# Optimization experiments

Hardware: AMD Instinct MI355X
Metric: run time of the kernel (lower is better)

Reference implementation:

```python
import jax, jax.numpy as jnp
import numpy as np
import math

B, L, D = 4, 4096, 64

def setup_inputs() -> dict:
    key = jax.random.key(0)
    kq, kk, kv = jax.random.split(key, 3)
    q = jax.random.normal(kq, (B, L, D), dtype=jnp.float32)
    k = jax.random.normal(kk, (B, L, D), dtype=jnp.float32)
    v = jax.random.normal(kv, (B, L, D), dtype=jnp.float32)
    return {"q": q, "k": k, "v": v}

def reference(q, k, v):
    d_model = k.shape[-1]
    # score[b,i,j] = <q_i, k_j> / sqrt(d)   -> [B, L, L]
    score = jnp.einsum('bid,bjd->bij', q, k) / math.sqrt(d_model)
    attn = jax.nn.softmax(score.astype(jnp.float32), axis=-1)
    # Faithful to source: output = (v^T @ attn)^T = attn^T @ v
    # output[b,j,d] = sum_i attn[b,i,j] * v[b,i,d]
    out = jnp.einsum('bij,bid->bjd', attn, v)
    return out
```

## Files before the change

kernel.cpp:

```cpp
#include <hip/hip_runtime.h>
#include <hip/hip_bf16.h>

#define LQ 4096
#define DD 64
#define NB 4
#define NTOT ((size_t)NB * LQ * DD)
#define NROW ((size_t)NB * LQ)

typedef __attribute__((ext_vector_type(4))) float f32x4;
typedef __attribute__((ext_vector_type(8))) short short8;
typedef __attribute__((ext_vector_type(2))) unsigned int uint2v;
typedef __attribute__((ext_vector_type(4))) unsigned short ushort4v;

static __device__ __forceinline__ unsigned short f2bf(float x) {
  __hip_bfloat16 h = __float2bfloat16(x);
  return __builtin_bit_cast(unsigned short, h);
}
static __device__ __forceinline__ float bf2f(unsigned short u) {
  unsigned int v = ((unsigned int)u) << 16;
  return __builtin_bit_cast(float, v);
}
static __device__ __forceinline__ float ex2(float x) { return __builtin_amdgcn_exp2f(x); }

static __device__ __forceinline__ void gl_lds16(const unsigned short* g, unsigned short* l) {
  __builtin_amdgcn_global_load_lds(
      (const __attribute__((address_space(1))) unsigned int*)g,
      (__attribute__((address_space(3))) unsigned int*)l, 16, 0, 0);
}

#define C1 0.18033688011112042f

__global__ __launch_bounds__(256) void prep_kernel(
    const float* __restrict__ q, const float* __restrict__ k,
    const float* __restrict__ v,
    unsigned short* __restrict__ Qb, unsigned short* __restrict__ Kb,
    unsigned short* __restrict__ Vb)
{
  const int arr = blockIdx.x >> 9;
  const size_t off = (((size_t)(blockIdx.x & 511)) * 256 + threadIdx.x) * 8;
  const float* s = arr == 0 ? q : arr == 1 ? k : v;
  unsigned short* d = arr == 0 ? Qb : arr == 1 ? Kb : Vb;
  const f32x4 x0 = *(const f32x4*)(s + off);
  const f32x4 x1 = *(const f32x4*)(s + off + 4);
  ushort4v o0 = { f2bf(x0[0]), f2bf(x0[1]), f2bf(x0[2]), f2bf(x0[3]) };
  ushort4v o1 = { f2bf(x1[0]), f2bf(x1[1]), f2bf(x1[2]), f2bf(x1[3]) };
  *(ushort4v*)(d + off) = o0;
  *(ushort4v*)(d + off + 4) = o1;
}

__global__ __launch_bounds__(256, 2) void stats_kernel(
    const unsigned short* __restrict__ Qb, const unsigned short* __restrict__ Kb,
    float* __restrict__ part_ls)
{
  __shared__ __align__(16) unsigned short stK[3][2048];
  const int bx = blockIdx.x;
  const int jc = bx & 7, it = (bx >> 3) & 15, b = bx >> 7;
  const int tid = threadIdx.x, w = tid >> 6, lane = tid & 63;
  const int l15 = lane & 15, g = lane >> 4;
  const int i0 = it * 256 + w * 64;
  const int jbase = jc * 512;
  const unsigned short* Kbase = Kb + (size_t)b * LQ * DD;

  short8 aq[4][2];
#pragma unroll
  for (int is = 0; is < 4; ++is)
#pragma unroll
    for (int kh = 0; kh < 2; ++kh)
      aq[is][kh] = *(const short8*)(Qb + ((size_t)b * LQ + i0 + is * 16 + l15) * DD + kh * 32 + g * 8);

  float ls[4][4];
#pragma unroll
  for (int is = 0; is < 4; ++is)
#pragma unroll
    for (int qq = 0; qq < 4; ++qq) ls[is][qq] = 0.f;

  const int srow = w * 8 + (lane >> 3);
  const int scol = ((lane & 7) ^ (lane >> 3)) << 3;

  gl_lds16(Kbase + (size_t)(jbase + srow) * DD + scol, &stK[0][w * 512]);
  gl_lds16(Kbase + (size_t)(jbase + 32 + srow) * DD + scol, &stK[1][w * 512]);
  asm volatile("s_waitcnt vmcnt(1)" ::: "memory");
  __builtin_amdgcn_s_barrier();

  for (int itr = 0; itr < 16; ++itr) {
    const int cur = itr % 3;
    const int tn = (itr + 2 < 16) ? itr + 2 : 15;
    gl_lds16(Kbase + (size_t)(jbase + tn * 32 + srow) * DD + scol, &stK[(itr + 2) % 3][w * 512]);

    short8 kf[2][2];
#pragma unroll
    for (int jsub = 0; jsub < 2; ++jsub)
#pragma unroll
      for (int kh = 0; kh < 2; ++kh) {
        const int row = jsub * 16 + l15;
        kf[jsub][kh] = *(const short8*)(&stK[cur][row * 64 + (((kh * 4 + g) ^ (l15 & 7)) << 3)]);
      }
#pragma unroll
    for (int is = 0; is < 4; ++is)
#pragma unroll
      for (int jsub = 0; jsub < 2; ++jsub) {
        f32x4 tt = __builtin_amdgcn_mfma_f32_16x16x32_bf16(
            aq[is][0], kf[jsub][0], (f32x4){0.f, 0.f, 0.f, 0.f}, 0, 0, 0);
        tt = __builtin_amdgcn_mfma_f32_16x16x32_bf16(aq[is][1], kf[jsub][1], tt, 0, 0, 0);
#pragma unroll
        for (int qq = 0; qq < 4; ++qq) ls[is][qq] += ex2(tt[qq] * C1);
      }
    asm volatile("s_waitcnt vmcnt(1)" ::: "memory");
    __builtin_amdgcn_s_barrier();
  }
#pragma unroll
  for (int mask = 1; mask <= 8; mask <<= 1)
#pragma unroll
    for (int is = 0; is < 4; ++is)
#pragma unroll
      for (int qq = 0; qq < 4; ++qq) ls[is][qq] += __shfl_xor(ls[is][qq], mask, 64);
  if (l15 == 0) {
#pragma unroll
    for (int is = 0; is < 4; ++is)
#pragma unroll
      for (int qq = 0; qq < 4; ++qq)
        part_ls[(size_t)jc * NROW + b * LQ + i0 + is * 16 + g * 4 + qq] = ls[is][qq];
  }
}

__global__ __launch_bounds__(256) void combine_kernel(
    const float* __restrict__ part_ls, const unsigned short* __restrict__ Vb,
    unsigned short* __restrict__ Vs)
{
  const size_t base = ((size_t)blockIdx.x * 256 + threadIdx.x) * 8;
  const int r = (int)(base >> 6);
  float l = 0.f;
#pragma unroll
  for (int jc = 0; jc < 8; ++jc) l += part_ls[(size_t)jc * NROW + r];
  const float s = 1.0f / l;
  const ushort4v a = *(const ushort4v*)(Vb + base);
  const ushort4v c = *(const ushort4v*)(Vb + base + 4);
  ushort4v oa = { f2bf(bf2f(a[0]) * s), f2bf(bf2f(a[1]) * s),
                  f2bf(bf2f(a[2]) * s), f2bf(bf2f(a[3]) * s) };
  ushort4v oc = { f2bf(bf2f(c[0]) * s), f2bf(bf2f(c[1]) * s),
                  f2bf(bf2f(c[2]) * s), f2bf(bf2f(c[3]) * s) };
  *(ushort4v*)(Vs + base) = oa;
  *(ushort4v*)(Vs + base + 4) = oc;
}

__global__ __launch_bounds__(1024, 4) void attn_out_kernel(
    const unsigned short* __restrict__ Qb, const unsigned short* __restrict__ Kb,
    const unsigned short* __restrict__ Vs, float* __restrict__ out)
{
  __shared__ __align__(16) unsigned short stage[16][4096];
  __shared__ __align__(16) unsigned short Pall[16 * 544];

  const int bx = blockIdx.x;
  const int jt = bx & 63;
  const int b  = bx >> 6;
  const int tid = threadIdx.x, w = tid >> 6, lane = tid & 63;
  const int p = w >> 1, sub = w & 1;
  const int l15 = lane & 15, g = lane >> 4;
  const int j0 = jt * 64 + sub * 32;

  const unsigned short* Qbase = Qb + (size_t)b * LQ * DD;
  const unsigned short* Vbase = Vs + (size_t)b * LQ * DD;

  short8 ka[2][2];
#pragma unroll
  for (int jsl = 0; jsl < 2; ++jsl)
#pragma unroll
    for (int kh = 0; kh < 2; ++kh)
      ka[jsl][kh] = *(const short8*)(Kb + ((size_t)b * LQ + j0 + jsl * 16 + l15) * DD + kh * 32 + g * 8);

  f32x4 acc[2][4];
#pragma unroll
  for (int jsl = 0; jsl < 2; ++jsl)
#pragma unroll
    for (int ds = 0; ds < 4; ++ds) acc[jsl][ds] = (f32x4){0.f, 0.f, 0.f, 0.f};

  const int ibase = p * 512;
  const int qrow = lane >> 3;
  const int qcol = ((lane & 7) ^ (lane >> 3)) << 3;
  const int vrow = (lane >> 5) * 4 + ((lane >> 1) & 3);
  const int vcol = (((lane >> 3) & 3) << 4) + ((lane & 1) << 3);

  unsigned short* Pw = &Pall[w * 544];
  const unsigned pbyte = (unsigned)(size_t)Pw;
  const unsigned sbyte = (unsigned)(size_t)&stage[w][0];

#define STAGE(I0) do { \
    _Pragma("unroll") \
    for (int kk = 0; kk < 4; ++kk) { \
      gl_lds16(Qbase + (size_t)((I0) + kk * 8 + qrow) * DD + qcol, &stage[w][kk * 512]); \
      gl_lds16(Vbase + (size_t)((I0) + kk * 8 + vrow) * DD + vcol, &stage[w][2048 + kk * 512]); \
    } \
  } while (0)

  STAGE(ibase);
  asm volatile("s_waitcnt vmcnt(0)" ::: "memory");

  for (int itr = 0; itr < 16; ++itr) {
    short8 qf[2][2];
#pragma unroll
    for (int is = 0; is < 2; ++is)
#pragma unroll
      for (int kh = 0; kh < 2; ++kh) {
        const int row = is * 16 + l15;
        qf[is][kh] = *(const short8*)(&stage[w][row * 64 + (((kh * 4 + g) ^ (l15 & 7)) << 3)]);
      }

    unsigned long long v0, v1, v2, v3, v4, v5, v6, v7;
    const unsigned av = sbyte + 4096 + g * 1024 + l15 * 8;
    asm volatile(
        "ds_read_b64_tr_b16 %0, %8\n\t"
        "ds_read_b64_tr_b16 %1, %8 offset:512\n\t"
        "ds_read_b64_tr_b16 %2, %8 offset:128\n\t"
        "ds_read_b64_tr_b16 %3, %8 offset:640\n\t"
        "ds_read_b64_tr_b16 %4, %8 offset:256\n\t"
        "ds_read_b64_tr_b16 %5, %8 offset:768\n\t"
        "ds_read_b64_tr_b16 %6, %8 offset:384\n\t"
        "ds_read_b64_tr_b16 %7, %8 offset:896\n\t"
        "s_waitcnt lgkmcnt(0)"
        : "=&v"(v0), "=&v"(v1), "=&v"(v2), "=&v"(v3),
          "=&v"(v4), "=&v"(v5), "=&v"(v6), "=&v"(v7)
        : "v"(av) : "memory");
    union U { unsigned long long u[2]; short8 s; };
    U vf0, vf1, vf2, vf3;
    vf0.u[0] = v0; vf0.u[1] = v1;
    vf1.u[0] = v2; vf1.u[1] = v3;
    vf2.u[0] = v4; vf2.u[1] = v5;
    vf3.u[0] = v6; vf3.u[1] = v7;

    if (itr + 1 < 16) STAGE(ibase + (itr + 1) * 32);

#pragma unroll
    for (int jsl = 0; jsl < 2; ++jsl) {
      __builtin_amdgcn_s_setprio(1);
#pragma unroll
      for (int is = 0; is < 2; ++is) {
        f32x4 tt = __builtin_amdgcn_mfma_f32_16x16x32_bf16(
            ka[jsl][0], qf[is][0], (f32x4){0.f, 0.f, 0.f, 0.f}, 0, 0, 0);
        tt = __builtin_amdgcn_mfma_f32_16x16x32_bf16(ka[jsl][1], qf[is][1], tt, 0, 0, 0);
        const unsigned a0 = __builtin_bit_cast(unsigned, ex2(tt[0] * C1)) + 0x8000u;
        const unsigned a1 = __builtin_bit_cast(unsigned, ex2(tt[1] * C1)) + 0x8000u;
        const unsigned a2 = __builtin_bit_cast(unsigned, ex2(tt[2] * C1)) + 0x8000u;
        const unsigned a3 = __builtin_bit_cast(unsigned, ex2(tt[3] * C1)) + 0x8000u;
        uint2v uu;
        uu[0] = __builtin_amdgcn_perm(a1, a0, 0x07060302u);
        uu[1] = __builtin_amdgcn_perm(a3, a2, 0x07060302u);
        const int il = is * 16 + l15;
        *(uint2v*)(&Pw[(il >> 2) * 68 + (il & 3) * 16 + g * 4]) = uu;
      }
      __builtin_amdgcn_s_setprio(0);

      unsigned long long p0, p1;
      const unsigned ap = pbyte + g * 272 + l15 * 8;
      asm volatile(
          "s_waitcnt lgkmcnt(0)\n\t"
          "ds_read_b64_tr_b16 %0, %2\n\t"
          "ds_read_b64_tr_b16 %1, %2 offset:136\n\t"
          "s_waitcnt lgkmcnt(0)"
          : "=&v"(p0), "=&v"(p1)
          : "v"(ap) : "memory");
      U pa;
      pa.u[0] = p0; pa.u[1] = p1;
      __builtin_amdgcn_s_setprio(1);
      acc[jsl][0] = __builtin_amdgcn_mfma_f32_16x16x32_bf16(pa.s, vf0.s, acc[jsl][0], 0, 0, 0);
      acc[jsl][1] = __builtin_amdgcn_mfma_f32_16x16x32_bf16(pa.s, vf1.s, acc[jsl][1], 0, 0, 0);
      acc[jsl][2] = __builtin_amdgcn_mfma_f32_16x16x32_bf16(pa.s, vf2.s, acc[jsl][2], 0, 0, 0);
      acc[jsl][3] = __builtin_amdgcn_mfma_f32_16x16x32_bf16(pa.s, vf3.s, acc[jsl][3], 0, 0, 0);
      __builtin_amdgcn_s_setprio(0);
    }

    asm volatile("s_waitcnt vmcnt(0)" ::: "memory");
  }
#undef STAGE

  __syncthreads();
  float* red = (float*)&stage[0][0];
#pragma unroll
  for (int jsl = 0; jsl < 2; ++jsl)
#pragma unroll
    for (int ds = 0; ds < 4; ++ds)
#pragma unroll
      for (int qq = 0; qq < 4; ++qq)
        red[w * 2048 + (jsl * 16 + g * 4 + qq) * 64 + ds * 16 + l15] = acc[jsl][ds][qq];
  __syncthreads();
  {
    float* op = out + ((size_t)b * LQ + jt * 64) * DD;
#pragma unroll
    for (int rr = 0; rr < 4; ++rr) {
      const int r = w * 4 + rr;
      const int sr = r >> 5, rl = r & 31;
      float s = 0.f;
#pragma unroll
      for (int pp = 0; pp < 8; ++pp)
        s += red[(pp * 2 + sr) * 2048 + rl * 64 + lane];
      op[r * 64 + lane] = s;
    }
  }
}

extern "C" void kernel_launch(void* const* d_in, const int* in_sizes, int n_in,
                              void* d_out, int out_size, void* d_ws, size_t ws_size,
                              hipStream_t stream) {
  const float* q = (const float*)d_in[0];
  const float* k = (const float*)d_in[1];
  const float* v = (const float*)d_in[2];

  unsigned short* Qb = (unsigned short*)d_ws;
  unsigned short* Kb = Qb + NTOT;
  unsigned short* Vb = Kb + NTOT;
  unsigned short* Vs = Vb + NTOT;
  float* part_ls = (float*)(Vs + NTOT);
  float* outp = (float*)d_out;

  prep_kernel<<<1536, 256, 0, stream>>>(q, k, v, Qb, Kb, Vb);
  stats_kernel<<<NB * 16 * 8, 256, 0, stream>>>(Qb, Kb, part_ls);
  combine_kernel<<<512, 256, 0, stream>>>(part_ls, Vb, Vs);
  attn_out_kernel<<<NB * 64, 1024, 0, stream>>>(Qb, Kb, Vs, outp);
}
```

Baseline: 60.79 us.

## Feed QK^T accumulator directly into PV MFMA, removing LDS P round-trip

Swaps the operand order of the score MFMA so its accumulator layout directly matches the A-operand layout of 16x16x16 bf16 MFMAs. The probabilities are packed in registers and used straight away, dropping the per-wave LDS write and transposed read of P along with their waitcnt stalls. V staging and the transposed V reads are re-laid out to match the new K=16 fragment shape. In exchange, the PV product now issues twice as many smaller MFMAs (16x16x16 instead of 16x16x32).

After: 59.73 us. About the same (-1.8%).

```diff
diff --git a/kernel.cpp b/kernel.cpp
--- a/kernel.cpp
+++ b/kernel.cpp
@@ -9,6 +9,7 @@
 
 typedef __attribute__((ext_vector_type(4))) float f32x4;
 typedef __attribute__((ext_vector_type(8))) short short8;
+typedef __attribute__((ext_vector_type(4))) short short4v;
 typedef __attribute__((ext_vector_type(2))) unsigned int uint2v;
 typedef __attribute__((ext_vector_type(4))) unsigned short ushort4v;
 
@@ -21,6 +22,16 @@
   return __builtin_bit_cast(float, v);
 }
 static __device__ __forceinline__ float ex2(float x) { return __builtin_amdgcn_exp2f(x); }
+
+static __device__ __forceinline__ f32x4 mfma16(short4v a, short4v b, f32x4 c) {
+#if __has_builtin(__builtin_amdgcn_mfma_f32_16x16x16bf16_1k)
+  return __builtin_amdgcn_mfma_f32_16x16x16bf16_1k(a, b, c, 0, 0, 0);
+#else
+  asm volatile("v_mfma_f32_16x16x16_bf16 %0, %1, %2, %0"
+               : "+v"(c) : "v"(a), "v"(b));
+  return c;
+#endif
+}
 
 static __device__ __forceinline__ void gl_lds16(const unsigned short* g, unsigned short* l) {
   __builtin_amdgcn_global_load_lds(
@@ -148,7 +159,6 @@
     const unsigned short* __restrict__ Vs, float* __restrict__ out)
 {
   __shared__ __align__(16) unsigned short stage[16][4096];
-  __shared__ __align__(16) unsigned short Pall[16 * 544];
 
   const int bx = blockIdx.x;
   const int jt = bx & 63;
@@ -177,18 +187,17 @@
   const int ibase = p * 512;
   const int qrow = lane >> 3;
   const int qcol = ((lane & 7) ^ (lane >> 3)) << 3;
-  const int vrow = (lane >> 5) * 4 + ((lane >> 1) & 3);
-  const int vcol = (((lane >> 3) & 3) << 4) + ((lane & 1) << 3);
-
-  unsigned short* Pw = &Pall[w * 544];
-  const unsigned pbyte = (unsigned)(size_t)Pw;
+  const int vgr = ((lane & 31) >> 3) * 4 + ((lane & 7) >> 1);
+  const int vdc = (lane >> 5) * 16 + (lane & 1) * 8;
+
   const unsigned sbyte = (unsigned)(size_t)&stage[w][0];
 
 #define STAGE(I0) do { \
     _Pragma("unroll") \
     for (int kk = 0; kk < 4; ++kk) { \
       gl_lds16(Qbase + (size_t)((I0) + kk * 8 + qrow) * DD + qcol, &stage[w][kk * 512]); \
-      gl_lds16(Vbase + (size_t)((I0) + kk * 8 + vrow) * DD + vcol, &stage[w][2048 + kk * 512]); \
+      gl_lds16(Vbase + (size_t)((I0) + (kk >> 1) * 16 + vgr) * DD + (kk & 1) * 32 + vdc, \
+               &stage[w][2048 + kk * 512]); \
     } \
   } while (0)
 
@@ -206,37 +215,41 @@
       }
 
     unsigned long long v0, v1, v2, v3, v4, v5, v6, v7;
-    const unsigned av = sbyte + 4096 + g * 1024 + l15 * 8;
+    const unsigned av = sbyte + 4096 + g * 128 + l15 * 8;
     asm volatile(
         "ds_read_b64_tr_b16 %0, %8\n\t"
         "ds_read_b64_tr_b16 %1, %8 offset:512\n\t"
-        "ds_read_b64_tr_b16 %2, %8 offset:128\n\t"
-        "ds_read_b64_tr_b16 %3, %8 offset:640\n\t"
-        "ds_read_b64_tr_b16 %4, %8 offset:256\n\t"
-        "ds_read_b64_tr_b16 %5, %8 offset:768\n\t"
-        "ds_read_b64_tr_b16 %6, %8 offset:384\n\t"
-        "ds_read_b64_tr_b16 %7, %8 offset:896\n\t"
+        "ds_read_b64_tr_b16 %2, %8 offset:1024\n\t"
+        "ds_read_b64_tr_b16 %3, %8 offset:1536\n\t"
+        "ds_read_b64_tr_b16 %4, %8 offset:2048\n\t"
+        "ds_read_b64_tr_b16 %5, %8 offset:2560\n\t"
+        "ds_read_b64_tr_b16 %6, %8 offset:3072\n\t"
+        "ds_read_b64_tr_b16 %7, %8 offset:3584\n\t"
         "s_waitcnt lgkmcnt(0)"
         : "=&v"(v0), "=&v"(v1), "=&v"(v2), "=&v"(v3),
           "=&v"(v4), "=&v"(v5), "=&v"(v6), "=&v"(v7)
         : "v"(av) : "memory");
-    union U { unsigned long long u[2]; short8 s; };
-    U vf0, vf1, vf2, vf3;
-    vf0.u[0] = v0; vf0.u[1] = v1;
-    vf1.u[0] = v2; vf1.u[1] = v3;
-    vf2.u[0] = v4; vf2.u[1] = v5;
-    vf3.u[0] = v6; vf3.u[1] = v7;
+    short4v vf[2][4];
+    vf[0][0] = __builtin_bit_cast(short4v, v0);
+    vf[0][1] = __builtin_bit_cast(short4v, v1);
+    vf[0][2] = __builtin_bit_cast(short4v, v2);
+    vf[0][3] = __builtin_bit_cast(short4v, v3);
+    vf[1][0] = __builtin_bit_cast(short4v, v4);
+    vf[1][1] = __builtin_bit_cast(short4v, v5);
+    vf[1][2] = __builtin_bit_cast(short4v, v6);
+    vf[1][3] = __builtin_bit_cast(short4v, v7);
 
     if (itr + 1 < 16) STAGE(ibase + (itr + 1) * 32);
 
 #pragma unroll
     for (int jsl = 0; jsl < 2; ++jsl) {
+      short4v pa[2];
       __builtin_amdgcn_s_setprio(1);
 #pragma unroll
       for (int is = 0; is < 2; ++is) {
         f32x4 tt = __builtin_amdgcn_mfma_f32_16x16x32_bf16(
-            ka[jsl][0], qf[is][0], (f32x4){0.f, 0.f, 0.f, 0.f}, 0, 0, 0);
-        tt = __builtin_amdgcn_mfma_f32_16x16x32_bf16(ka[jsl][1], qf[is][1], tt, 0, 0, 0);
+            qf[is][0], ka[jsl][0], (f32x4){0.f, 0.f, 0.f, 0.f}, 0, 0, 0);
+        tt = __builtin_amdgcn_mfma_f32_16x16x32_bf16(qf[is][1], ka[jsl][1], tt, 0, 0, 0);
         const unsigned a0 = __builtin_bit_cast(unsigned, ex2(tt[0] * C1)) + 0x8000u;
         const unsigned a1 = __builtin_bit_cast(unsigned, ex2(tt[1] * C1)) + 0x8000u;
         const unsigned a2 = __builtin_bit_cast(unsigned, ex2(tt[2] * C1)) + 0x8000u;
@@ -244,27 +257,15 @@
         uint2v uu;
         uu[0] = __builtin_amdgcn_perm(a1, a0, 0x07060302u);
         uu[1] = __builtin_amdgcn_perm(a3, a2, 0x07060302u);
-        const int il = is * 16 + l15;
-        *(uint2v*)(&Pw[(il >> 2) * 68 + (il & 3) * 16 + g * 4]) = uu;
-      }
-      __builtin_amdgcn_s_setprio(0);
-
-      unsigned long long p0, p1;
-      const unsigned ap = pbyte + g * 272 + l15 * 8;
-      asm volatile(
-          "s_waitcnt lgkmcnt(0)\n\t"
-          "ds_read_b64_tr_b16 %0, %2\n\t"
-          "ds_read_b64_tr_b16 %1, %2 offset:136\n\t"
-          "s_waitcnt lgkmcnt(0)"
-          : "=&v"(p0), "=&v"(p1)
-          : "v"(ap) : "memory");
-      U pa;
-      pa.u[0] = p0; pa.u[1] = p1;
-      __builtin_amdgcn_s_setprio(1);
-      acc[jsl][0] = __builtin_amdgcn_mfma_f32_16x16x32_bf16(pa.s, vf0.s, acc[jsl][0], 0, 0, 0);
-      acc[jsl][1] = __builtin_amdgcn_mfma_f32_16x16x32_bf16(pa.s, vf1.s, acc[jsl][1], 0, 0, 0);
-      acc[jsl][2] = __builtin_amdgcn_mfma_f32_16x16x32_bf16(pa.s, vf2.s, acc[jsl][2], 0, 0, 0);
-      acc[jsl][3] = __builtin_amdgcn_mfma_f32_16x16x32_bf16(pa.s, vf3.s, acc[jsl][3], 0, 0, 0);
+        pa[is] = __builtin_bit_cast(short4v, uu);
+      }
+#pragma unroll
+      for (int is = 0; is < 2; ++is) {
+        acc[jsl][0] = mfma16(pa[is], vf[is][0], acc[jsl][0]);
+        acc[jsl][1] = mfma16(pa[is], vf[is][1], acc[jsl][1]);
+        acc[jsl][2] = mfma16(pa[is], vf[is][2], acc[jsl][2]);
+        acc[jsl][3] = mfma16(pa[is], vf[is][3], acc[jsl][3]);
+      }
       __builtin_amdgcn_s_setprio(0);
     }
 
```
